# Optimization experiments

Hardware: AMD Instinct MI355X
Metric: run time of the kernel (lower is better)

## Reference

```python
import jax, jax.numpy as jnp
import numpy as np

LEAK = 0.2

def leaky(x):
    return jnp.where(x > 0, x, LEAK * x)

def relu(x):
    return jnp.maximum(x, 0)

def conv1d(x, w):
    # x [B,Cin,L], w [Cout,Cin,3], stride 1, padding 1
    return jax.lax.conv_general_dilated(x, w, (1,), [(1, 1)],
        dimension_numbers=('NCH', 'OIH', 'NCH'))

def conv2d(x, w, pad, dil=1, groups=1):
    return jax.lax.conv_general_dilated(x, w, (1, 1), [(pad, pad), (pad, pad)],
        rhs_dilation=(dil, dil), feature_group_count=groups,
        dimension_numbers=('NCHW', 'OIHW', 'NCHW'))

def bn2d(x, p, eps=1e-5):
    # p: [4,C] = gamma, beta, running_mean, running_var (eval-mode BN)
    g, b, m, v = p
    s = (1, -1, 1, 1)
    return (x - m.reshape(s)) * (g.reshape(s) / jnp.sqrt(v.reshape(s) + eps)) + b.reshape(s)

def layernorm(x, g, b, eps=1e-5):
    mu = x.mean(-1, keepdims=True)
    var = ((x - mu) ** 2).mean(-1, keepdims=True)
    return (x - mu) / jnp.sqrt(var + eps) * g + b

def l2n(x, axis, eps):
    n = jnp.sqrt((x * x).sum(axis, keepdims=True))
    return x / jnp.maximum(n, eps)


def setup_inputs() -> dict:
    key = jax.random.key(0)
    B, C, H, W = 4, 64, 48, 48
    D, Fn, T, V = 256, 8, 4, 16
    E = 16  # orthogonal prototype embed dim
    ks = iter(jax.random.split(key, 64))
    def rn(shape, s=0.05):
        return jax.random.normal(next(ks), shape, jnp.float32) * s
    def bnp(c):
        return jnp.stack([1.0 + rn((c,), 0.1), rn((c,), 0.1), rn((c,), 0.1), 1.0 + jnp.abs(rn((c,), 0.1))])
    return dict(
        basis_vector_bank=jax.random.normal(next(ks), (T, V, D), jnp.float32),
        task_f=jax.random.normal(next(ks), (B, C, 16, 16), jnp.float32),
        img_f=jax.random.normal(next(ks), (B, C, H, W), jnp.float32),
        protos=jax.random.normal(next(ks), (T, E), jnp.float32),
        tA_w1=rn((E // 4, 1, 3)), tA_w2=rn((E // 2, E // 4, 3)),
        iA_w=rn((E // 2, C, 3, 3)), iA_bn=bnp(E // 2),
        at_w1=rn((E, Fn // 2 * E)), at_b1=rn((Fn // 2 * E,)),
        at_ln_g=jnp.ones((Fn // 2 * E,)), at_ln_b=jnp.zeros((Fn // 2 * E,)),
        at_w2=rn((Fn // 2 * E, Fn * E)), at_b2=rn((Fn * E,)),
        bv_t1=rn((D // 4, 1, 3)), bv_t2=rn((D // 2, D // 4, 3)),
        bv_ic1=rn((D // 4, C, 3, 3)), bv_bn1=bnp(D // 4),
        bv_ic2=rn((D // 2, D // 4, 3, 3)), bv_bn2=bnp(D // 2),
        bv_w1=rn((D, D // 4)), bv_b1=rn((D // 4,)),
        bv_ln_g=jnp.ones((D // 4,)), bv_ln_b=jnp.zeros((D // 4,)),
        bv_w2=rn((D // 4, D)), bv_b2=rn((D,)),
        m1_w1=rn((D, D // 4)), m1_b1=rn((D // 4,)),
        m1_ln_g=jnp.ones((D // 4,)), m1_ln_b=jnp.zeros((D // 4,)),
        m1_w2=rn((D // 4, C * C)), m1_b2=rn((C * C,)),
        m3_w1=rn((D, D // 4)), m3_b1=rn((D // 4,)),
        m3_ln_g=jnp.ones((D // 4,)), m3_ln_b=jnp.zeros((D // 4,)),
        m3_w2=rn((D // 4, 9 * C * C)), m3_b2=rn((9 * C * C,)),
        blr_bn=bnp(C),
        zc_w=rn((C, C, 1, 1), 0.01), zc_b=rn((C,), 0.01),
    )


def _forward(basis_vector_bank, task_f, img_f, protos, tA_w1, tA_w2, iA_w, iA_bn,
             at_w1, at_b1, at_ln_g, at_ln_b, at_w2, at_b2,
             bv_t1, bv_t2, bv_ic1, bv_bn1, bv_ic2, bv_bn2,
             bv_w1, bv_b1, bv_ln_g, bv_ln_b, bv_w2, bv_b2,
             m1_w1, m1_b1, m1_ln_g, m1_ln_b, m1_w2, m1_b2,
             m3_w1, m3_b1, m3_ln_g, m3_ln_b, m3_w2, m3_b2,
             blr_bn, zc_w, zc_b):
    T, V, D = basis_vector_bank.shape
    B, C, H, W = img_f.shape
    E = protos.shape[1]
    Fn = at_w2.shape[1] // E
    tau = 0.5

    # --- A2SI routing features ---
    xt = task_f.reshape(B, 1, -1)
    t1 = conv1d(leaky(conv1d(xt, tA_w1)), tA_w2).mean(-1)          # [B,E/2]
    i1 = leaky(bn2d(conv2d(img_f, iA_w, 1), iA_bn)).mean((2, 3))   # [B,E/2]
    f1 = jnp.concatenate([t1, i1], axis=1)                         # [B,E]
    h = relu(layernorm(f1 @ at_w1 + at_b1, at_ln_g, at_ln_b))
    tif = (h @ at_w2 + at_b2).reshape(B, E, Fn)                    # [B,E,F]
    logits = jnp.einsum('te,bef->bft', l2n(protos, -1, 1e-8), l2n(tif, 1, 1e-8))  # [B,F,T]

    # hard gumbel-softmax (straight-through), fixed noise key for determinism
    u = jax.random.uniform(jax.random.key(42), logits.shape, jnp.float32, 1e-10, 1.0)
    g = -jnp.log(-jnp.log(u))
    y = jax.nn.softmax((logits + g) / tau, axis=-1)
    idx = jnp.argmax(y, axis=-1)                                   # [B,F]
    y_hard = jax.nn.one_hot(idx, T, dtype=y.dtype)
    set_type = y_hard + y - jax.lax.stop_gradient(y)

    bank_flat = basis_vector_bank.reshape(T, V * D)
    sbvb = jnp.einsum('bft,tk->bfk', set_type, bank_flat).reshape(B, Fn, V, D)

    # --- BasisV_filter: filter feature ---
    xt2 = task_f.reshape(B, C, -1)
    rms = jnp.sqrt((xt2 ** 2).mean((1, 2), keepdims=True))
    xt2 = (xt2 / (rms + 1e-8)).reshape(B, 1, -1)
    te = conv1d(leaky(conv1d(xt2, bv_t1)), bv_t2).mean(-1)         # [B,D/2]
    ie = leaky(bn2d(conv2d(img_f, bv_ic1, 1), bv_bn1))
    ie = leaky(bn2d(conv2d(ie, bv_ic2, 1), bv_bn2)).mean((2, 3))   # [B,D/2]
    ff = jnp.concatenate([te, ie], axis=1)                         # [B,D]
    ff = relu(layernorm(ff @ bv_w1 + bv_b1, bv_ln_g, bv_ln_b)) @ bv_w2 + bv_b2

    # --- per-(batch,type) group gather/top-k/scatter, vectorized ---
    # group bank = bank of first filter with that type (hard one-hot -> type's bank)
    occ = idx[:, None, :] == jnp.arange(T)[None, :, None]          # [B,T,F]
    first = jnp.argmax(occ, axis=-1)                               # [B,T]
    Bg = jnp.take_along_axis(sbvb, first[:, :, None, None], axis=1)  # [B,T,V,D]
    # all rows of Q within a group are identical (filter_f expanded over F),
    # so S.max(0) == cosine(ff[b], Bg[b,t])
    scores = jnp.einsum('bd,btvd->btv', l2n(ff, -1, 1e-12), l2n(Bg, -1, 1e-12))
    order = jnp.argsort(-scores, axis=-1)                          # [B,T,V] topk order
    lt = jnp.tril(jnp.ones((Fn, Fn), bool), -1)                    # j < i
    rank = ((idx[:, :, None] == idx[:, None, :]) & lt).sum(-1)     # position in group
    bidx = jnp.arange(B)[:, None]
    sel = order[bidx, idx, rank]                                   # [B,F]
    bvf = Bg[bidx, idx, sel]                                       # [B,F,D]

    # --- per-filter dynamic convolutions ---
    w1 = relu(layernorm(bvf @ m1_w1 + m1_b1, m1_ln_g, m1_ln_b)) @ m1_w2 + m1_b2
    w1 = w1.reshape(B, Fn, C, C)                                   # [B,F,out,in]
    w3 = relu(layernorm(bvf @ m3_w1 + m3_b1, m3_ln_g, m3_ln_b)) @ m3_w2 + m3_b2
    w3 = w3.reshape(B * Fn, C, C, 3, 3)

    dp0 = jnp.einsum('bfoc,bchw->bfohw', w1, img_f)                # 1x1 branch
    xin = jnp.broadcast_to(img_f[:, None], (B, Fn, C, H, W)).reshape(1, B * Fn * C, H, W)
    ker = w3.reshape(B * Fn * C, C, 3, 3)
    dpd = [conv2d(xin, ker, d, dil=d, groups=B * Fn).reshape(B, Fn, C, H, W)
           for d in (1, 2, 3)]                                     # same-padded dilated 3x3
    t_ = idx[:, :, None, None, None]
    dp = jnp.where(t_ == 0, dp0, jnp.where(t_ == 1, dpd[0],
         jnp.where(t_ == 2, dpd[1], dpd[2])))                      # [B,F,C,H,W]

    x = leaky(bn2d(dp.reshape(B * Fn, C, H, W), blr_bn)).reshape(B, Fn, C, H, W).mean(1)
    a = conv2d(x, zc_w, 0) + zc_b.reshape(1, -1, 1, 1)
    return a + img_f


@jax.jit
def reference(basis_vector_bank, task_f, img_f, protos, tA_w1, tA_w2, iA_w, iA_bn,
              at_w1, at_b1, at_ln_g, at_ln_b, at_w2, at_b2,
              bv_t1, bv_t2, bv_ic1, bv_bn1, bv_ic2, bv_bn2,
              bv_w1, bv_b1, bv_ln_g, bv_ln_b, bv_w2, bv_b2,
              m1_w1, m1_b1, m1_ln_g, m1_ln_b, m1_w2, m1_b2,
              m3_w1, m3_b1, m3_ln_g, m3_ln_b, m3_w2, m3_b2,
              blr_bn, zc_w, zc_b):
    return _forward(basis_vector_bank, task_f, img_f, protos, tA_w1, tA_w2, iA_w, iA_bn,
                    at_w1, at_b1, at_ln_g, at_ln_b, at_w2, at_b2,
                    bv_t1, bv_t2, bv_ic1, bv_bn1, bv_ic2, bv_bn2,
                    bv_w1, bv_b1, bv_ln_g, bv_ln_b, bv_w2, bv_b2,
                    m1_w1, m1_b1, m1_ln_g, m1_ln_b, m1_w2, m1_b2,
                    m3_w1, m3_b1, m3_ln_g, m3_ln_b, m3_w2, m3_b2,
                    blr_bn, zc_w, zc_b)
```

## Files before the change

kernel.cpp:

```cpp
#include <hip/hip_runtime.h>
#include <math.h>

#define LEAKC 0.2f

#define NB 4
#define NC 64
#define LLEN 16384
#define HW 2304
#define PP 54
#define PHW 2916
#define SLABP 72

typedef __attribute__((ext_vector_type(8))) short short8;
typedef __attribute__((ext_vector_type(4))) float floatx4;

__device__ __forceinline__ float leaky(float x){ return x > 0.f ? x : LEAKC*x; }

__device__ __forceinline__ float wave_sum64(float v){
  for(int off=32;off;off>>=1) v += __shfl_xor(v,off);
  return v;
}

__device__ __forceinline__ unsigned short f2bf(float x){
  unsigned u=__float_as_uint(x);
  unsigned r=u+0x7FFFu+((u>>16)&1u);
  return (unsigned short)(r>>16);
}

__device__ __forceinline__ void threefry2x32(unsigned k0, unsigned k1, unsigned& x0, unsigned& x1){
  unsigned ks0=k0, ks1=k1, ks2=k0^k1^0x1BD11BDAu;
  x0+=ks0; x1+=ks1;
  const int rot0[4]={13,15,26,6};
  const int rot1[4]={17,29,16,24};
#define TF_APPLY(rr) {for(int r=0;r<4;r++){x0+=x1; x1=(x1<<rr[r])|(x1>>(32-rr[r])); x1^=x0;}}
  TF_APPLY(rot0); x0+=ks1; x1+=ks2+1u;
  TF_APPLY(rot1); x0+=ks2; x1+=ks0+2u;
  TF_APPLY(rot0); x0+=ks0; x1+=ks1+3u;
  TF_APPLY(rot1); x0+=ks1; x1+=ks2+4u;
  TF_APPLY(rot0); x0+=ks2; x1+=ks0+5u;
#undef TF_APPLY
}

__device__ __forceinline__ float jax_uniform128(int i){
  unsigned x0=0u, x1=(unsigned)i;
  threefry2x32(0u,42u,x0,x1);
  unsigned bits = x0 ^ x1;
  unsigned fb=(bits>>9)|0x3f800000u;
  float f=__uint_as_float(fb)-1.0f;
  float u=f*(1.0f-1e-10f)+1e-10f;
  return fmaxf(1e-10f,u);
}

__global__ __launch_bounds__(256) void k_pre(const float* __restrict__ task_f,
                      const float* __restrict__ w1A, const float* __restrict__ w1B,
                      float* __restrict__ totA, float* __restrict__ a0A, float* __restrict__ aLA,
                      float* __restrict__ totB, float* __restrict__ a0B, float* __restrict__ aLB,
                      float* __restrict__ rmsacc,
                      const float* __restrict__ img,
                      const float* __restrict__ w1, const float* __restrict__ w2,
                      const float* __restrict__ wa,
                      unsigned short* __restrict__ imgTP,
                      unsigned short* __restrict__ W1T, unsigned short* __restrict__ W2T,
                      unsigned short* __restrict__ WAT,
                      const float* __restrict__ mw1, const float* __restrict__ mw3,
                      const float* __restrict__ bvw1p, const float* __restrict__ bvw2p,
                      const float* __restrict__ bvt2p, const float* __restrict__ atw2p,
                      const float* __restrict__ bankp, float* __restrict__ warm){
  if(blockIdx.x<256){
    int b=blockIdx.x>>6, seg=blockIdx.x&63;
    const float* x=task_f+b*LLEN;
    float tA[4]={0,0,0,0};
    float tB[64];
#pragma unroll
    for(int c=0;c<64;c++) tB[c]=0.f;
    float sq=0.f;
    int l=seg*256+threadIdx.x;
    {
      float xm=(l>0)?x[l-1]:0.f;
      float xc=x[l];
      float xp=(l<LLEN-1)?x[l+1]:0.f;
      sq=xc*xc;
#pragma unroll
      for(int c=0;c<4;c++){
        float a=leaky(w1A[c*3+0]*xm + w1A[c*3+1]*xc + w1A[c*3+2]*xp);
        tA[c]=a;
        if(l==0) a0A[b*4+c]=a;
        if(l==LLEN-1) aLA[b*4+c]=a;
      }
#pragma unroll
      for(int c=0;c<64;c++){
        float a=leaky(w1B[c*3+0]*xm + w1B[c*3+1]*xc + w1B[c*3+2]*xp);
        tB[c]=a;
        if(l==0) a0B[b*64+c]=a;
        if(l==LLEN-1) aLB[b*64+c]=a;
      }
    }
    sq=wave_sum64(sq);
#pragma unroll
    for(int c=0;c<4;c++) tA[c]=wave_sum64(tA[c]);
#pragma unroll
    for(int c=0;c<64;c++){
      float v=tB[c];
      for(int off=32;off;off>>=1) v+=__shfl_down(v,off);
      tB[c]=v;
    }
    __shared__ float redB[4][64];
    __shared__ float redA[4][4];
    __shared__ float redQ[4];
    int wave=threadIdx.x>>6, lane=threadIdx.x&63;
    if(lane==0){
#pragma unroll
      for(int c=0;c<64;c++) redB[wave][c]=tB[c];
#pragma unroll
      for(int c=0;c<4;c++) redA[wave][c]=tA[c];
      redQ[wave]=sq;
    }
    __syncthreads();
    if(threadIdx.x<64){
      float s=redB[0][threadIdx.x]+redB[1][threadIdx.x]+redB[2][threadIdx.x]+redB[3][threadIdx.x];
      atomicAdd(&totB[b*64+threadIdx.x], s);
    } else if(threadIdx.x<68){
      int c=threadIdx.x-64;
      float s=redA[0][c]+redA[1][c]+redA[2][c]+redA[3][c];
      atomicAdd(&totA[b*4+c], s);
    } else if(threadIdx.x==68){
      atomicAdd(&rmsacc[b], redQ[0]+redQ[1]+redQ[2]+redQ[3]);
    }
  } else if(blockIdx.x<400){
    int blk=blockIdx.x-256;
    int b=blk/36, t=blk%36;
    int p0=t*64;
    __shared__ float tile[64][65];
    int pp=threadIdx.x&63, c4=threadIdx.x>>6;
    for(int r=0;r<16;r++){
      int c=c4*16+r;
      tile[c][pp]=img[(b*64+c)*HW + p0+pp];
    }
    __syncthreads();
    int pxl=threadIdx.x>>2, cg=(threadIdx.x&3)*16;
    unsigned out[8];
#pragma unroll
    for(int q=0;q<8;q++){
      unsigned lo=f2bf(tile[cg+2*q][pxl]);
      unsigned hi=f2bf(tile[cg+2*q+1][pxl]);
      out[q]=lo|(hi<<16);
    }
    int px=p0+pxl;
    int h=px/48, w=px-h*48;
    int poff=(h+3)*PP+(w+3);
    unsigned* dst=(unsigned*)(imgTP + ((size_t)(b*PHW+poff))*64 + cg);
#pragma unroll
    for(int q=0;q<8;q++) dst[q]=out[q];
  } else if(blockIdx.x<868){
    int n=(blockIdx.x-400)*256+threadIdx.x;
    if(n<9*64*64){
      int tap=n>>12, oc=(n>>6)&63, c=n&63;
      W1T[n]=f2bf(w1[oc*576+c*9+tap]);
    } else if(n<9*64*64+9*128*64){
      int m=n-9*64*64;
      int tap=m/8192, r=m-tap*8192, oc=r>>6, c=r&63;
      W2T[m]=f2bf(w2[oc*576+c*9+tap]);
    } else {
      int q=n-9*64*64-9*128*64;
      if(q<9*16*64){
        int tap=q>>10, r=q&1023, o=r>>6, c=r&63;
        WAT[q]=(o<8)?f2bf(wa[o*576+c*9+tap]):(unsigned short)0;
      }
    }
  } else {
    int t=(blockIdx.x-868)*256+threadIdx.x;
    float a=0.f;
    for(int i=t;i*16<16384;i+=4096) a+=mw1[i*16];
    for(int i=t;i*16<16384;i+=4096) a+=mw3[i*16];
    for(int i=t;i*16<16384;i+=4096) a+=bvw1p[i*16];
    for(int i=t;i*16<16384;i+=4096) a+=bvw2p[i*16];
    for(int i=t;i*16<24576;i+=4096) a+=bvt2p[i*16];
    for(int i=t;i*16<8192;i+=4096) a+=atw2p[i*16];
    for(int i=t;i*16<16384;i+=4096) a+=bankp[i*16];
    warm[t&1023]=a;
  }
}

__global__ __launch_bounds__(256) void k_conv1(const unsigned short* __restrict__ imgTP,
                        const unsigned short* __restrict__ W1T,
                        const unsigned short* __restrict__ WAT,
                        const float* __restrict__ bn1, const float* __restrict__ bnA,
                        unsigned short* __restrict__ ie1TP, float* __restrict__ i1){
  int lane=threadIdx.x&63, mt=threadIdx.x>>6;
  int n0=lane&15, kg=lane>>4;
  if(blockIdx.x<96){
    int blk=blockIdx.x;
    int b=blk/24, hp=blk-b*24;
    int h0=hp*2;
    __shared__ unsigned short slab[4*54*SLABP];
    {
      const unsigned short* ibase=imgTP+((size_t)b*PHW+(size_t)(h0+2)*PP)*64;
      for(int e=threadIdx.x;e<4*54*8;e+=256){
        int rr=e/(54*8), rem=e-rr*54*8, w=rem>>3, ck=rem&7;
        uint4 v=*(const uint4*)(ibase+((size_t)(rr*PP+w))*64+ck*8);
        *(uint4*)(slab+(rr*54+w)*SLABP+ck*8)=v;
      }
    }
    __syncthreads();
    floatx4 acc[6];
#pragma unroll
    for(int i=0;i<6;i++) acc[i]=(floatx4){0.f,0.f,0.f,0.f};
#pragma unroll
    for(int ti=0;ti<3;ti++){
#pragma unroll
      for(int tj=0;tj<3;tj++){
        int tap=ti*3+tj;
        const unsigned short* Ab=W1T+(size_t)tap*4096;
#pragma unroll
        for(int c0=0;c0<64;c0+=32){
          short8 a=*(const short8*)(Ab+((mt*16+n0)*64+c0+kg*8));
#pragma unroll
          for(int rr=0;rr<2;rr++){
            int sr=rr+ti;
#pragma unroll
            for(int wc=0;wc<3;wc++){
              int wp=wc*16+n0+tj+2;
              short8 bv=*(const short8*)(slab+(sr*54+wp)*SLABP+c0+kg*8);
              acc[rr*3+wc]=__builtin_amdgcn_mfma_f32_16x16x32_bf16(a,bv,acc[rr*3+wc],0,0,0);
            }
          }
        }
      }
    }
    int obase=mt*16+kg*4;
    float scale[4],m_[4],be_[4];
#pragma unroll
    for(int reg=0;reg<4;reg++){
      int o=obase+reg;
      scale[reg]=bn1[o]/sqrtf(bn1[192+o]+1e-5f);
      m_[reg]=bn1[128+o]; be_[reg]=bn1[64+o];
    }
#pragma unroll
    for(int rr=0;rr<2;rr++){
#pragma unroll
      for(int wc=0;wc<3;wc++){
        int poff=(h0+rr+3)*PP + wc*16+n0+3;
        float v0=leaky((acc[rr*3+wc][0]-m_[0])*scale[0]+be_[0]);
        float v1=leaky((acc[rr*3+wc][1]-m_[1])*scale[1]+be_[1]);
        float v2=leaky((acc[rr*3+wc][2]-m_[2])*scale[2]+be_[2]);
        float v3=leaky((acc[rr*3+wc][3]-m_[3])*scale[3]+be_[3]);
        unsigned w0=f2bf(v0)|((unsigned)f2bf(v1)<<16);
        unsigned w1=f2bf(v2)|((unsigned)f2bf(v3)<<16);
        uint2 pk={w0,w1};
        *(uint2*)(ie1TP+((size_t)(b*PHW+poff)*64+obase))=pk;
      }
    }
  } else {
    int blk=blockIdx.x-96;
    int b=blk/6, hg=blk%6;
    int hp=hg*4+mt;
    int h0=hp*2;
    const unsigned short* ib=imgTP+(size_t)b*PHW*64;
    floatx4 acc[6];
#pragma unroll
    for(int i=0;i<6;i++) acc[i]=(floatx4){0.f,0.f,0.f,0.f};
#pragma unroll
    for(int ti=0;ti<3;ti++){
#pragma unroll
      for(int tj=0;tj<3;tj++){
        int tap=ti*3+tj;
        const unsigned short* Ab=WAT+(size_t)tap*1024;
#pragma unroll
        for(int c0=0;c0<64;c0+=32){
          short8 a=*(const short8*)(Ab+(n0*64+c0+kg*8));
#pragma unroll
          for(int rr=0;rr<2;rr++){
            int r=h0+rr+ti-1+3;
#pragma unroll
            for(int wc=0;wc<3;wc++){
              int w=wc*16+n0+tj-1+3;
              short8 bv=*(const short8*)(ib+((size_t)(r*PP+w)*64+c0+kg*8));
              acc[rr*3+wc]=__builtin_amdgcn_mfma_f32_16x16x32_bf16(a,bv,acc[rr*3+wc],0,0,0);
            }
          }
        }
      }
    }
    int obase=kg*4;
#pragma unroll
    for(int reg=0;reg<4;reg++){
      int o=obase+reg;
      float part=0;
      if(o<8){
        float scale=bnA[o]/sqrtf(bnA[24+o]+1e-5f);
        float m_=bnA[16+o], be_=bnA[8+o];
#pragma unroll
        for(int i=0;i<6;i++) part+=leaky((acc[i][reg]-m_)*scale+be_);
      }
      for(int off=1;off<16;off<<=1) part+=__shfl_xor(part,off);
      if(n0==0 && o<8) atomicAdd(&i1[b*8+o], part*(1.f/2304.f));
    }
  }
}

__global__ __launch_bounds__(512) void k_ic2M(const unsigned short* __restrict__ ie1TP,
                       const unsigned short* __restrict__ W2T,
                       const float* __restrict__ bn, float* __restrict__ ie){
  int blk=blockIdx.x;
  int b=blk/24, hp=blk-b*24;
  int tid=threadIdx.x;
  int lane=tid&63, mt=tid>>6;
  int n0=lane&15, kg=lane>>4;
  int h0=hp*2;
  __shared__ unsigned short slab[4*54*SLABP];
  {
    const unsigned short* ibase=ie1TP+((size_t)b*PHW+(size_t)(h0+2)*PP)*64;
    for(int e=tid;e<4*54*8;e+=512){
      int rr=e/(54*8), rem=e-rr*54*8, w=rem>>3, ck=rem&7;
      uint4 v=*(const uint4*)(ibase+((size_t)(rr*PP+w))*64+ck*8);
      *(uint4*)(slab+(rr*54+w)*SLABP+ck*8)=v;
    }
  }
  __syncthreads();
  floatx4 acc[6];
#pragma unroll
  for(int i=0;i<6;i++) acc[i]=(floatx4){0.f,0.f,0.f,0.f};
#pragma unroll
  for(int ti=0;ti<3;ti++){
#pragma unroll
    for(int tj=0;tj<3;tj++){
      int tap=ti*3+tj;
      const unsigned short* Ab=W2T+(size_t)tap*8192;
#pragma unroll
      for(int c0=0;c0<64;c0+=32){
        short8 a=*(const short8*)(Ab+((mt*16+n0)*64+c0+kg*8));
#pragma unroll
        for(int rr=0;rr<2;rr++){
          int sr=rr+ti;
#pragma unroll
          for(int wc=0;wc<3;wc++){
            int wp=wc*16+n0+tj+2;
            short8 bv=*(const short8*)(slab+(sr*54+wp)*SLABP+c0+kg*8);
            acc[rr*3+wc]=__builtin_amdgcn_mfma_f32_16x16x32_bf16(a,bv,acc[rr*3+wc],0,0,0);
          }
        }
      }
    }
  }
  int obase=mt*16+kg*4;
#pragma unroll
  for(int reg=0;reg<4;reg++){
    int o=obase+reg;
    float scale=bn[o]/sqrtf(bn[384+o]+1e-5f);
    float m_=bn[256+o], be_=bn[128+o];
    float part=0;
#pragma unroll
    for(int i=0;i<6;i++) part+=leaky((acc[i][reg]-m_)*scale+be_);
    for(int off=1;off<16;off<<=1) part+=__shfl_xor(part,off);
    if(n0==0) atomicAdd(&ie[b*128+o], part*(1.f/2304.f));
  }
}

__global__ __launch_bounds__(512,1) void k_mid(
    const float* __restrict__ totA, const float* __restrict__ a0A, const float* __restrict__ aLA,
    const float* __restrict__ totB, const float* __restrict__ a0B, const float* __restrict__ aLB,
    const float* __restrict__ rmsacc,
    const float* __restrict__ tA_w2, const float* __restrict__ bv_t2,
    const float* __restrict__ i1, const float* __restrict__ ie,
    const float* __restrict__ at_w1, const float* __restrict__ at_b1,
    const float* __restrict__ at_ln_g, const float* __restrict__ at_ln_b,
    const float* __restrict__ at_w2, const float* __restrict__ at_b2,
    const float* __restrict__ protos,
    const float* __restrict__ bv_w1, const float* __restrict__ bv_b1,
    const float* __restrict__ bv_ln_g, const float* __restrict__ bv_ln_b,
    const float* __restrict__ bv_w2, const float* __restrict__ bv_b2,
    const float* __restrict__ bank,
    const float* __restrict__ m1_w1, const float* __restrict__ m1_b1,
    const float* __restrict__ m1_g,  const float* __restrict__ m1_bb,
    const float* __restrict__ m3_w1, const float* __restrict__ m3_b1,
    const float* __restrict__ m3_g,  const float* __restrict__ m3_bb,
    int* __restrict__ idxo, float* __restrict__ hid1, float* __restrict__ hid3){
  int b=blockIdx.x;
  int tid=threadIdx.x;
  int lane=tid&63, wv=tid>>6;
  const float invL=1.0f/16384.0f;
  __shared__ float sT[64], s0[64], sL[64];
  __shared__ float part[512];
  __shared__ float te_s[128], t1_s[8];
  __shared__ float f1[16], h[64], tif[128], tifn[128], tden[8], pden[4], pn[64], z[32];
  __shared__ int sidx[8], sfirst[4], srank[8], rows[8];
  __shared__ float fbuf[256], hh[64], ffn_s[256], finv_s;
  __shared__ float scores[64];
  __shared__ int order[64];
  __shared__ float bvf[2048];

  if(tid<64){ sT[tid]=totB[b*64+tid]; s0[tid]=a0B[b*64+tid]; sL[tid]=aLB[b*64+tid]; }
  __syncthreads();
  float scB=1.0f/(sqrtf(rmsacc[b]*invL)+1e-8f);
  if(tid<256){
    int c2=tid&127, h2=tid>>7;
    const float* wr=bv_t2+c2*192;
    float s=0;
    for(int c1=h2*32;c1<h2*32+32;c1+=8){
      float4 q[6];
      const float4* r4=(const float4*)(wr+c1*3);
#pragma unroll
      for(int u=0;u<6;u++) q[u]=r4[u];
      const float* qq=(const float*)q;
#pragma unroll
      for(int u=0;u<8;u++){
        int c=c1+u;
        float T=sT[c], A0=s0[c], AL=sL[c];
        s += qq[u*3+0]*(T-AL) + qq[u*3+1]*T + qq[u*3+2]*(T-A0);
      }
    }
    part[tid]=s;
  } else if(tid>=384 && tid<392){
    int c2=tid-384;
    float s=0;
    for(int c1=0;c1<4;c1++){
      float T=totA[b*4+c1], A0=a0A[b*4+c1], AL=aLA[b*4+c1];
      const float* w=&tA_w2[(c2*4+c1)*3];
      s += w[0]*(T-AL) + w[1]*T + w[2]*(T-A0);
    }
    t1_s[c2]=s*invL;
  }
  __syncthreads();
  if(tid<128) te_s[tid]=(part[tid]+part[tid+128])*invL*scB;
  __syncthreads();

  if(tid<8) f1[tid]=t1_s[tid];
  else if(tid<16) f1[tid]=i1[b*8+tid-8];
  __syncthreads();
  if(tid<64){
    float s=at_b1[lane];
#pragma unroll
    for(int i=0;i<16;i++) s+=f1[i]*at_w1[i*64+lane];
    float mu=wave_sum64(s)*(1.f/64.f);
    float d=s-mu;
    float var=wave_sum64(d*d)*(1.f/64.f);
    h[lane]=fmaxf(d*(1.0f/sqrtf(var+1e-5f))*at_ln_g[lane]+at_ln_b[lane],0.f);
  }
  __syncthreads();
  if(tid<256){
    int n=tid&127, h2=tid>>7;
    float a0=0,a1=0;
    for(int k=h2*32;k<h2*32+32;k+=2){
      a0+=h[k]*at_w2[k*128+n];
      a1+=h[k+1]*at_w2[(k+1)*128+n];
    }
    part[tid]=a0+a1;
  }
  __syncthreads();
  if(tid<128) tif[tid]=at_b2[tid]+part[tid]+part[tid+128];
  __syncthreads();
  if(tid<8){
    int f=tid;
    float ss=0; for(int e=0;e<16;e++){float v=tif[e*8+f]; ss+=v*v;}
    tden[f]=fmaxf(sqrtf(ss),1e-8f);
  } else if(tid<12){
    int t=tid-8;
    float ss=0; for(int e=0;e<16;e++){float v=protos[t*16+e]; ss+=v*v;}
    pden[t]=fmaxf(sqrtf(ss),1e-8f);
  }
  __syncthreads();
  if(tid<128) tifn[tid]=tif[tid]/tden[tid&7];
  if(tid<64) pn[tid]=protos[tid]/pden[tid>>4];
  __syncthreads();
  if(tid<32){
    int f=tid>>2, t=tid&3;
    float ss=0;
#pragma unroll
    for(int e=0;e<16;e++) ss+=pn[t*16+e]*tifn[e*8+f];
    float u=jax_uniform128(b*32+f*4+t);
    float g=-logf(-logf(u));
    z[tid]=ss+g;
  }
  __syncthreads();
  if(tid<8){
    float best=z[tid*4]; int bi=0;
    for(int t=1;t<4;t++){ float v=z[tid*4+t]; if(v>best){best=v;bi=t;} }
    sidx[tid]=bi;
  }
  __syncthreads();
  if(tid<4){
    int t=tid;
    int fi=0;
    for(int f=7;f>=0;f--) if(sidx[f]==t) fi=f;
    sfirst[t]=fi;
  } else if(tid<12){
    int f=tid-4;
    int c=0; for(int f2=0;f2<f;f2++) if(sidx[f2]==sidx[f]) c++;
    srank[f]=c;
  }
  __syncthreads();

  if(tid<128) fbuf[tid]=te_s[tid];
  else if(tid<256) fbuf[tid]=ie[b*128+tid-128];
  __syncthreads();
  if(tid<256){
    int l64=tid&63, q=tid>>6;
    float a0=0,a1=0,a2=0,a3=0;
    for(int k=q*64;k<q*64+64;k+=4){
      a0+=fbuf[k]  *bv_w1[k*64+l64];
      a1+=fbuf[k+1]*bv_w1[(k+1)*64+l64];
      a2+=fbuf[k+2]*bv_w1[(k+2)*64+l64];
      a3+=fbuf[k+3]*bv_w1[(k+3)*64+l64];
    }
    part[tid]=((a0+a1)+(a2+a3));
  }
  __syncthreads();
  if(tid<64){
    float s=bv_b1[lane]+part[lane]+part[64+lane]+part[128+lane]+part[192+lane];
    float mu=wave_sum64(s)*(1.f/64.f);
    float d=s-mu;
    float var=wave_sum64(d*d)*(1.f/64.f);
    hh[lane]=fmaxf(d*(1.0f/sqrtf(var+1e-5f))*bv_ln_g[lane]+bv_ln_b[lane],0.f);
  }
  __syncthreads();
  {
    int n=tid&255, h2=tid>>8;
    float a0=0,a1=0;
    for(int k=h2*32;k<h2*32+32;k+=2){
      a0+=hh[k]*bv_w2[k*256+n];
      a1+=hh[k+1]*bv_w2[(k+1)*256+n];
    }
    part[tid]=a0+a1;
  }
  __syncthreads();
  if(tid<256) ffn_s[tid]=bv_b2[tid]+part[tid]+part[tid+256];
  __syncthreads();
  if(tid<64){
    float sq=0;
#pragma unroll
    for(int u=0;u<4;u++){ float v=ffn_s[u*64+lane]; sq+=v*v; }
    sq=wave_sum64(sq);
    if(lane==0) finv_s=1.0f/fmaxf(sqrtf(sq),1e-12f);
  }
  __syncthreads();
  if(tid<256) ffn_s[tid]*=finv_s;
  __syncthreads();

  if(tid<128){
    int it=tid&63, h2=tid>>6;
    int t=it>>4, v=it&15;
    int tt=sidx[sfirst[t]];
    const float4* row=(const float4*)(bank+(tt*16+v)*256);
    float sa=0,na=0;
    for(int d4=h2*32;d4<h2*32+32;d4++){
      float4 r=row[d4];
      const float* fp=&ffn_s[d4*4];
      sa+=fp[0]*r.x+fp[1]*r.y+fp[2]*r.z+fp[3]*r.w;
      na+=r.x*r.x+r.y*r.y+r.z*r.z+r.w*r.w;
    }
    part[tid]=sa;
    part[256+tid]=na;
  }
  __syncthreads();
  if(tid<64) scores[tid]=(part[tid]+part[tid+64])/fmaxf(sqrtf(part[256+tid]+part[320+tid]),1e-12f);
  __syncthreads();
  if(tid<4){
    const float* sc=&scores[tid*16];
    unsigned used=0;
    for(int pk=0;pk<16;pk++){
      int best=-1; float bv=-1e30f;
      for(int v2=0;v2<16;v2++){
        if(used&(1u<<v2)) continue;
        float vv=sc[v2];
        if(best<0||vv>bv){bv=vv;best=v2;}
      }
      used|=1u<<best;
      order[tid*16+pk]=best;
    }
  }
  __syncthreads();
  if(tid<8){
    int t=sidx[tid];
    int v=order[t*16+srank[tid]];
    rows[tid]=t*16+v;
    idxo[b*8+tid]=t;
  }
  __syncthreads();

  for(int ii=tid;ii<2048;ii+=512){
    int r=ii>>8, d=ii&255;
    bvf[ii]=bank[rows[r]*256+d];
  }
  __syncthreads();
  {
    int r=wv;
    const float* bp=&bvf[r*256];
    float a0=0,a1=0,a2=0,a3=0;
    float c0=0,c1=0,c2=0,c3=0;
    for(int d=0;d<256;d+=4){
      float b0=bp[d],b1=bp[d+1],b2=bp[d+2],b3=bp[d+3];
      a0+=b0*m1_w1[d*64+lane];
      a1+=b1*m1_w1[(d+1)*64+lane];
      a2+=b2*m1_w1[(d+2)*64+lane];
      a3+=b3*m1_w1[(d+3)*64+lane];
      c0+=b0*m3_w1[d*64+lane];
      c1+=b1*m3_w1[(d+1)*64+lane];
      c2+=b2*m3_w1[(d+2)*64+lane];
      c3+=b3*m3_w1[(d+3)*64+lane];
    }
    float s1=m1_b1[lane]+((a0+a1)+(a2+a3));
    float s3=m3_b1[lane]+((c0+c1)+(c2+c3));
    float mu=wave_sum64(s1)*(1.f/64.f);
    float dd=s1-mu;
    float var=wave_sum64(dd*dd)*(1.f/64.f);
    hid1[(b*8+r)*64+lane]=fmaxf(dd*(1.0f/sqrtf(var+1e-5f))*m1_g[lane]+m1_bb[lane],0.f);
    mu=wave_sum64(s3)*(1.f/64.f);
    dd=s3-mu;
    var=wave_sum64(dd*dd)*(1.f/64.f);
    hid3[(b*8+r)*64+lane]=fmaxf(dd*(1.0f/sqrtf(var+1e-5f))*m3_g[lane]+m3_bb[lane],0.f);
  }
}

__global__ __launch_bounds__(256) void k_heads(const float* __restrict__ hid1, const float* __restrict__ hid3,
                        const float* __restrict__ w2a, const float* __restrict__ b2a,
                        const float* __restrict__ w2b, const float* __restrict__ b2b,
                        unsigned short* __restrict__ A1, unsigned short* __restrict__ A3){
  __shared__ float hl[2048];
  if(blockIdx.x<16){
    int n=blockIdx.x*256+threadIdx.x;
    for(int i=threadIdx.x;i<2048;i+=256) hl[i]=hid1[i];
    __syncthreads();
    float wcol[64];
#pragma unroll
    for(int k=0;k<64;k++) wcol[k]=w2a[k*4096+n];
    float bb=b2a[n];
    for(int bf=0;bf<32;bf++){
      float s=bb;
#pragma unroll
      for(int k=0;k<64;k++) s+=hl[bf*64+k]*wcol[k];
      A1[bf*4096+n]=f2bf(s);
    }
  } else {
    int n=(blockIdx.x-16)*256+threadIdx.x;
    for(int i=threadIdx.x;i<2048;i+=256) hl[i]=hid3[i];
    __syncthreads();
    float wcol[64];
#pragma unroll
    for(int k=0;k<64;k++) wcol[k]=w2b[(size_t)k*36864+n];
    float bb=b2b[n];
    int o=n/576, rem=n-o*576;
    int c=rem/9, tap=rem-c*9;
    size_t base=((size_t)tap*64+o)*64+c;
    for(int bf=0;bf<32;bf++){
      float s=bb;
#pragma unroll
      for(int k=0;k<64;k++) s+=hl[bf*64+k]*wcol[k];
      A3[(size_t)bf*9*4096+base]=f2bf(s);
    }
  }
}

__global__ __launch_bounds__(512) void k_dynF(const unsigned short* __restrict__ imgTP,
                       const unsigned short* __restrict__ A1, const unsigned short* __restrict__ A3,
                       const int* __restrict__ idx, const float* __restrict__ bn,
                       const float* __restrict__ zc_w, const float* __restrict__ zc_b,
                       const float* __restrict__ img, float* __restrict__ out){
  int blk=blockIdx.x;
  int b=blk/48, r0=blk-b*48;
  int tid=threadIdx.x;
  int lane=tid&63, w8=tid>>6;
  int mt=w8&3, fh=w8>>2;
  int n0=lane&15, kg=lane>>4;
  __shared__ unsigned short slab[7*54*SLABP];
  __shared__ float xl[64*50];
  __shared__ float zl[4096];
  for(int i=tid;i<4096;i+=512) zl[i]=zc_w[i];
  for(int i=tid;i<3200;i+=512) xl[i]=0.f;
  {
    const unsigned short* ibase=imgTP+((size_t)b*PHW+(size_t)r0*PP)*64;
    for(int e=tid;e<7*54*8;e+=512){
      int rr=e/(54*8), rem=e-rr*54*8, w=rem>>3, ck=rem&7;
      uint4 v=*(const uint4*)(ibase + ((size_t)(rr*PP+w))*64 + ck*8);
      *(uint4*)(slab + (rr*54+w)*SLABP + ck*8)=v;
    }
  }
  __syncthreads();
  int obase=mt*16+kg*4;
  float scale[4],m_[4],be_[4];
#pragma unroll
  for(int reg=0;reg<4;reg++){
    int o=obase+reg;
    scale[reg]=bn[o]/sqrtf(bn[192+o]+1e-5f);
    m_[reg]=bn[128+o]; be_[reg]=bn[64+o];
  }
  float xsum[3][4];
#pragma unroll
  for(int wc=0;wc<3;wc++)
#pragma unroll
    for(int reg=0;reg<4;reg++) xsum[wc][reg]=0.f;
  for(int f=fh*4;f<fh*4+4;f++){
    int bf=b*8+f;
    int tt=idx[bf];
    floatx4 acc[3];
#pragma unroll
    for(int i=0;i<3;i++) acc[i]=(floatx4){0.f,0.f,0.f,0.f};
    if(tt==0){
      const unsigned short* Ab=A1+(size_t)bf*4096;
#pragma unroll
      for(int c0=0;c0<64;c0+=32){
        short8 a=*(const short8*)(Ab+((mt*16+n0)*64+c0+kg*8));
#pragma unroll
        for(int wc=0;wc<3;wc++){
          short8 bv=*(const short8*)(slab + (3*54 + wc*16+n0+3)*SLABP + c0+kg*8);
          acc[wc]=__builtin_amdgcn_mfma_f32_16x16x32_bf16(a,bv,acc[wc],0,0,0);
        }
      }
    } else {
      int d=tt;
      const unsigned short* A3b=A3+(size_t)bf*9*4096;
#pragma unroll
      for(int ti=0;ti<3;ti++){
        int lr=d*(ti-1)+3;
#pragma unroll
        for(int tj=0;tj<3;tj++){
          int tap=ti*3+tj;
          int dw=d*(tj-1)+3;
          const unsigned short* Ab=A3b+(size_t)tap*4096;
#pragma unroll
          for(int c0=0;c0<64;c0+=32){
            short8 a=*(const short8*)(Ab+((mt*16+n0)*64+c0+kg*8));
#pragma unroll
            for(int wc=0;wc<3;wc++){
              short8 bv=*(const short8*)(slab + (lr*54 + wc*16+n0+dw)*SLABP + c0+kg*8);
              acc[wc]=__builtin_amdgcn_mfma_f32_16x16x32_bf16(a,bv,acc[wc],0,0,0);
            }
          }
        }
      }
    }
#pragma unroll
    for(int wc=0;wc<3;wc++)
#pragma unroll
      for(int reg=0;reg<4;reg++)
        xsum[wc][reg]+=leaky((acc[wc][reg]-m_[reg])*scale[reg]+be_[reg]);
  }
#pragma unroll
  for(int wc=0;wc<3;wc++)
#pragma unroll
    for(int reg=0;reg<4;reg++)
      atomicAdd(&xl[(obase+reg)*50 + wc*16+n0], xsum[wc][reg]*0.125f);
  __syncthreads();
  size_t base=(size_t)b*64*HW + r0*48;
  for(int e=tid;e<3072;e+=512){
    int o=e/48, px=e-o*48;
    float s=zc_b[o];
#pragma unroll
    for(int c=0;c<64;c++) s+=zl[o*64+c]*xl[c*50+px];
    size_t a=base+(size_t)o*HW+px;
    out[a]=s+img[a];
  }
}

extern "C" void kernel_launch(void* const* d_in, const int* in_sizes, int n_in,
                              void* d_out, int out_size, void* d_ws, size_t ws_size,
                              hipStream_t stream){
  const float* bank   =(const float*)d_in[0];
  const float* task_f =(const float*)d_in[1];
  const float* img_f  =(const float*)d_in[2];
  const float* protos =(const float*)d_in[3];
  const float* tA_w1  =(const float*)d_in[4];
  const float* tA_w2  =(const float*)d_in[5];
  const float* iA_w   =(const float*)d_in[6];
  const float* iA_bn  =(const float*)d_in[7];
  const float* at_w1  =(const float*)d_in[8];
  const float* at_b1  =(const float*)d_in[9];
  const float* at_ln_g=(const float*)d_in[10];
  const float* at_ln_b=(const float*)d_in[11];
  const float* at_w2  =(const float*)d_in[12];
  const float* at_b2  =(const float*)d_in[13];
  const float* bv_t1  =(const float*)d_in[14];
  const float* bv_t2  =(const float*)d_in[15];
  const float* bv_ic1 =(const float*)d_in[16];
  const float* bv_bn1 =(const float*)d_in[17];
  const float* bv_ic2 =(const float*)d_in[18];
  const float* bv_bn2 =(const float*)d_in[19];
  const float* bv_w1  =(const float*)d_in[20];
  const float* bv_b1  =(const float*)d_in[21];
  const float* bv_ln_g=(const float*)d_in[22];
  const float* bv_ln_b=(const float*)d_in[23];
  const float* bv_w2  =(const float*)d_in[24];
  const float* bv_b2  =(const float*)d_in[25];
  const float* m1_w1  =(const float*)d_in[26];
  const float* m1_b1  =(const float*)d_in[27];
  const float* m1_ln_g=(const float*)d_in[28];
  const float* m1_ln_b=(const float*)d_in[29];
  const float* m1_w2  =(const float*)d_in[30];
  const float* m1_b2  =(const float*)d_in[31];
  const float* m3_w1  =(const float*)d_in[32];
  const float* m3_b1  =(const float*)d_in[33];
  const float* m3_ln_g=(const float*)d_in[34];
  const float* m3_ln_b=(const float*)d_in[35];
  const float* m3_w2  =(const float*)d_in[36];
  const float* m3_b2  =(const float*)d_in[37];
  const float* blr_bn =(const float*)d_in[38];
  const float* zc_w   =(const float*)d_in[39];
  const float* zc_b   =(const float*)d_in[40];

  float* ws=(float*)d_ws;
  float* totA=ws+0;       float* a0A=ws+16;      float* aLA=ws+32;
  float* totB=ws+48;      float* a0B=ws+304;     float* aLB=ws+560;
  float* rmsacc=ws+816;   float* i1 =ws+820;     float* ie =ws+852;
  int*   idxp  =(int*)(ws+2932);
  float* hid1=ws+3044;    float* hid3=ws+5092;
  unsigned short* A1p  =(unsigned short*)(ws+7140);
  unsigned short* A3p  =(unsigned short*)(ws+72676);
  unsigned short* imgTP=(unsigned short*)(ws+662500);
  unsigned short* ie1TP=(unsigned short*)(ws+1035748);
  unsigned short* W1Tp =(unsigned short*)(ws+1408996);
  unsigned short* W2Tp =(unsigned short*)(ws+1427428);
  unsigned short* WATp =(unsigned short*)(ws+1464292);
  float* warm =ws+1468900;

  hipMemsetAsync(ws, 0, 1364*sizeof(float), stream);
  hipMemsetAsync(imgTP, 0, 2*746496*sizeof(unsigned short), stream);

  k_pre<<<884,256,0,stream>>>(task_f, tA_w1, bv_t1,
                              totA, a0A, aLA, totB, a0B, aLB, rmsacc,
                              img_f, bv_ic1, bv_ic2, iA_w, imgTP, W1Tp, W2Tp, WATp,
                              m1_w1, m3_w1, bv_w1, bv_w2, bv_t2, at_w2, bank, warm);
  k_conv1<<<120,256,0,stream>>>(imgTP, W1Tp, WATp, bv_bn1, iA_bn, ie1TP, i1);
  k_ic2M<<<96,512,0,stream>>>(ie1TP, W2Tp, bv_bn2, ie);
  k_mid<<<4,512,0,stream>>>(totA,a0A,aLA,totB,a0B,aLB, rmsacc, tA_w2, bv_t2, i1, ie,
                            at_w1, at_b1, at_ln_g, at_ln_b, at_w2, at_b2, protos,
                            bv_w1, bv_b1, bv_ln_g, bv_ln_b, bv_w2, bv_b2, bank,
                            m1_w1, m1_b1, m1_ln_g, m1_ln_b,
                            m3_w1, m3_b1, m3_ln_g, m3_ln_b,
                            idxp, hid1, hid3);
  k_heads<<<160,256,0,stream>>>(hid1, hid3, m1_w2, m1_b2, m3_w2, m3_b2, A1p, A3p);
  k_dynF<<<192,512,0,stream>>>(imgTP, A1p, A3p, idxp, blr_bn, zc_w, zc_b, img_f, (float*)d_out);

  (void)in_sizes; (void)n_in; (void)out_size; (void)ws_size;
}
```

Before: 284.4 us.

## Fuse two conv stages in LDS and replace atomics with partial-sum buffers

Merges the first and second 3x3 convolutions into one kernel. The intermediate activation stays in shared memory with a one-row halo that is recomputed per block, so the global ie1TP round trip and one launch go away. Atomic accumulations in k_pre and the conv kernels become per-block partial writes that k_mid sums, which removes both hipMemsetAsync calls. Only the imgTP padding border is zeroed, by extra blocks inside k_pre. The cost is about 50% redundant conv1 work for the halo rows, fewer blocks for the second conv, and serial reductions added to k_mid.

```diff
diff --git a/kernel.cpp b/kernel.cpp
--- a/kernel.cpp
+++ b/kernel.cpp
@@ -10,6 +10,8 @@
 #define PP 54
 #define PHW 2916
 #define SLABP 72
+#define CP 72
+#define IE1C 50
 
 typedef __attribute__((ext_vector_type(8))) short short8;
 typedef __attribute__((ext_vector_type(4))) float floatx4;
@@ -53,9 +55,9 @@
 
 __global__ __launch_bounds__(256) void k_pre(const float* __restrict__ task_f,
                       const float* __restrict__ w1A, const float* __restrict__ w1B,
-                      float* __restrict__ totA, float* __restrict__ a0A, float* __restrict__ aLA,
-                      float* __restrict__ totB, float* __restrict__ a0B, float* __restrict__ aLB,
-                      float* __restrict__ rmsacc,
+                      float* __restrict__ totApart, float* __restrict__ a0A, float* __restrict__ aLA,
+                      float* __restrict__ totBpart, float* __restrict__ a0B, float* __restrict__ aLB,
+                      float* __restrict__ rmspart,
                       const float* __restrict__ img,
                       const float* __restrict__ w1, const float* __restrict__ w2,
                       const float* __restrict__ wa,
@@ -118,13 +120,12 @@
     __syncthreads();
     if(threadIdx.x<64){
       float s=redB[0][threadIdx.x]+redB[1][threadIdx.x]+redB[2][threadIdx.x]+redB[3][threadIdx.x];
-      atomicAdd(&totB[b*64+threadIdx.x], s);
+      totBpart[(size_t)(b*64+seg)*64+threadIdx.x]=s;
     } else if(threadIdx.x<68){
       int c=threadIdx.x-64;
-      float s=redA[0][c]+redA[1][c]+redA[2][c]+redA[3][c];
-      atomicAdd(&totA[b*4+c], s);
+      totApart[(b*64+seg)*4+c]=redA[0][c]+redA[1][c]+redA[2][c]+redA[3][c];
     } else if(threadIdx.x==68){
-      atomicAdd(&rmsacc[b], redQ[0]+redQ[1]+redQ[2]+redQ[3]);
+      rmspart[b*64+seg]=redQ[0]+redQ[1]+redQ[2]+redQ[3];
     }
   } else if(blockIdx.x<400){
     int blk=blockIdx.x-256;
@@ -167,7 +168,7 @@
         WAT[q]=(o<8)?f2bf(wa[o*576+c*9+tap]):(unsigned short)0;
       }
     }
-  } else {
+  } else if(blockIdx.x<884){
     int t=(blockIdx.x-868)*256+threadIdx.x;
     float a=0.f;
     for(int i=t;i*16<16384;i+=4096) a+=mw1[i*16];
@@ -178,82 +179,148 @@
     for(int i=t;i*16<8192;i+=4096) a+=atw2p[i*16];
     for(int i=t;i*16<16384;i+=4096) a+=bankp[i*16];
     warm[t&1023]=a;
-  }
-}
-
-__global__ __launch_bounds__(256) void k_conv1(const unsigned short* __restrict__ imgTP,
+  } else {
+    int id=(blockIdx.x-884)*256+threadIdx.x;
+    uint4 z=make_uint4(0,0,0,0);
+    for(int cch=id;cch<19584;cch+=4096){
+      int ck=cch&7, pxid=cch>>3;
+      int b=pxid/612, p=pxid-b*612;
+      int h,w;
+      if(p<324){ int r=p/54; w=p-r*54; h=(r<3)?r:(r+48); }
+      else { int q=p-324; int r2=q/6; int cc=q-r2*6; h=3+r2; w=(cc<3)?cc:(cc+48); }
+      *(uint4*)(imgTP + ((size_t)(b*PHW + h*PP + w))*64 + ck*8)=z;
+    }
+  }
+}
+
+__global__ __launch_bounds__(512) void k_conv12(const unsigned short* __restrict__ imgTP,
                         const unsigned short* __restrict__ W1T,
+                        const unsigned short* __restrict__ W2T,
                         const unsigned short* __restrict__ WAT,
-                        const float* __restrict__ bn1, const float* __restrict__ bnA,
-                        unsigned short* __restrict__ ie1TP, float* __restrict__ i1){
-  int lane=threadIdx.x&63, mt=threadIdx.x>>6;
+                        const float* __restrict__ bn1, const float* __restrict__ bn2,
+                        const float* __restrict__ bnA,
+                        float* __restrict__ iepart, float* __restrict__ i1part){
+  int tid=threadIdx.x;
+  int lane=tid&63, wv=tid>>6;
   int n0=lane&15, kg=lane>>4;
   if(blockIdx.x<96){
     int blk=blockIdx.x;
     int b=blk/24, hp=blk-b*24;
     int h0=hp*2;
-    __shared__ unsigned short slab[4*54*SLABP];
+    __shared__ unsigned short slab[6*54*SLABP];
+    __shared__ unsigned short ie1[4*IE1C*CP];
     {
-      const unsigned short* ibase=imgTP+((size_t)b*PHW+(size_t)(h0+2)*PP)*64;
-      for(int e=threadIdx.x;e<4*54*8;e+=256){
+      const unsigned short* ibase=imgTP+((size_t)b*PHW+(size_t)(h0+1)*PP)*64;
+      for(int e=tid;e<6*54*8;e+=512){
         int rr=e/(54*8), rem=e-rr*54*8, w=rem>>3, ck=rem&7;
         uint4 v=*(const uint4*)(ibase+((size_t)(rr*PP+w))*64+ck*8);
         *(uint4*)(slab+(rr*54+w)*SLABP+ck*8)=v;
       }
+      if(tid<64){
+        int br=tid>>4, cq=(tid>>3)&1, ck=tid&7;
+        *(uint4*)(ie1+((size_t)(br*IE1C+(cq?49:0)))*CP+ck*8)=make_uint4(0,0,0,0);
+      }
     }
     __syncthreads();
-    floatx4 acc[6];
-#pragma unroll
-    for(int i=0;i<6;i++) acc[i]=(floatx4){0.f,0.f,0.f,0.f};
-#pragma unroll
-    for(int ti=0;ti<3;ti++){
-#pragma unroll
-      for(int tj=0;tj<3;tj++){
-        int tap=ti*3+tj;
-        const unsigned short* Ab=W1T+(size_t)tap*4096;
-#pragma unroll
-        for(int c0=0;c0<64;c0+=32){
-          short8 a=*(const short8*)(Ab+((mt*16+n0)*64+c0+kg*8));
-#pragma unroll
-          for(int rr=0;rr<2;rr++){
-            int sr=rr+ti;
-#pragma unroll
-            for(int wc=0;wc<3;wc++){
-              int wp=wc*16+n0+tj+2;
-              short8 bv=*(const short8*)(slab+(sr*54+wp)*SLABP+c0+kg*8);
-              acc[rr*3+wc]=__builtin_amdgcn_mfma_f32_16x16x32_bf16(a,bv,acc[rr*3+wc],0,0,0);
+    {
+      int mt=wv&3, rh=wv>>2;
+      floatx4 acc[2][3];
+#pragma unroll
+      for(int rr=0;rr<2;rr++)
+#pragma unroll
+        for(int nt=0;nt<3;nt++) acc[rr][nt]=(floatx4){0.f,0.f,0.f,0.f};
+#pragma unroll
+      for(int ti=0;ti<3;ti++){
+#pragma unroll
+        for(int tj=0;tj<3;tj++){
+          int tap=ti*3+tj;
+          const unsigned short* Ab=W1T+(size_t)tap*4096;
+#pragma unroll
+          for(int c0=0;c0<64;c0+=32){
+            short8 a=*(const short8*)(Ab+((mt*16+n0)*64+c0+kg*8));
+#pragma unroll
+            for(int rr=0;rr<2;rr++){
+              int sr=rh*2+rr+ti;
+#pragma unroll
+              for(int nt=0;nt<3;nt++){
+                int sc=nt*16+n0+tj+2;
+                short8 bv=*(const short8*)(slab+(sr*54+sc)*SLABP+c0+kg*8);
+                acc[rr][nt]=__builtin_amdgcn_mfma_f32_16x16x32_bf16(a,bv,acc[rr][nt],0,0,0);
+              }
             }
           }
         }
       }
-    }
-    int obase=mt*16+kg*4;
-    float scale[4],m_[4],be_[4];
-#pragma unroll
-    for(int reg=0;reg<4;reg++){
-      int o=obase+reg;
-      scale[reg]=bn1[o]/sqrtf(bn1[192+o]+1e-5f);
-      m_[reg]=bn1[128+o]; be_[reg]=bn1[64+o];
-    }
-#pragma unroll
-    for(int rr=0;rr<2;rr++){
-#pragma unroll
-      for(int wc=0;wc<3;wc++){
-        int poff=(h0+rr+3)*PP + wc*16+n0+3;
-        float v0=leaky((acc[rr*3+wc][0]-m_[0])*scale[0]+be_[0]);
-        float v1=leaky((acc[rr*3+wc][1]-m_[1])*scale[1]+be_[1]);
-        float v2=leaky((acc[rr*3+wc][2]-m_[2])*scale[2]+be_[2]);
-        float v3=leaky((acc[rr*3+wc][3]-m_[3])*scale[3]+be_[3]);
-        unsigned w0=f2bf(v0)|((unsigned)f2bf(v1)<<16);
-        unsigned w1=f2bf(v2)|((unsigned)f2bf(v3)<<16);
-        uint2 pk={w0,w1};
-        *(uint2*)(ie1TP+((size_t)(b*PHW+poff)*64+obase))=pk;
+      int obase=mt*16+kg*4;
+      float scale[4],m_[4],be_[4];
+#pragma unroll
+      for(int reg=0;reg<4;reg++){
+        int o=obase+reg;
+        scale[reg]=bn1[o]/sqrtf(bn1[192+o]+1e-5f);
+        m_[reg]=bn1[128+o]; be_[reg]=bn1[64+o];
+      }
+#pragma unroll
+      for(int rr=0;rr<2;rr++){
+        int br=rh*2+rr;
+        bool rv=((unsigned)(h0-1+br))<48u;
+#pragma unroll
+        for(int nt=0;nt<3;nt++){
+          float v0=rv?leaky((acc[rr][nt][0]-m_[0])*scale[0]+be_[0]):0.f;
+          float v1=rv?leaky((acc[rr][nt][1]-m_[1])*scale[1]+be_[1]):0.f;
+          float v2=rv?leaky((acc[rr][nt][2]-m_[2])*scale[2]+be_[2]):0.f;
+          float v3=rv?leaky((acc[rr][nt][3]-m_[3])*scale[3]+be_[3]):0.f;
+          unsigned w0=f2bf(v0)|((unsigned)f2bf(v1)<<16);
+          unsigned w1=f2bf(v2)|((unsigned)f2bf(v3)<<16);
+          uint2 pk={w0,w1};
+          *(uint2*)(ie1+((size_t)(br*IE1C+(nt*16+1+n0)))*CP+obase)=pk;
+        }
+      }
+    }
+    __syncthreads();
+    {
+      int mt2=wv;
+      floatx4 acc[6];
+#pragma unroll
+      for(int i=0;i<6;i++) acc[i]=(floatx4){0.f,0.f,0.f,0.f};
+#pragma unroll
+      for(int ti=0;ti<3;ti++){
+#pragma unroll
+        for(int tj=0;tj<3;tj++){
+          int tap=ti*3+tj;
+          const unsigned short* Ab=W2T+(size_t)tap*8192;
+#pragma unroll
+          for(int c0=0;c0<64;c0+=32){
+            short8 a=*(const short8*)(Ab+((mt2*16+n0)*64+c0+kg*8));
+#pragma unroll
+            for(int rr=0;rr<2;rr++){
+              int sr=rr+ti;
+#pragma unroll
+              for(int wc=0;wc<3;wc++){
+                int q=wc*16+n0+tj;
+                short8 bv=*(const short8*)(ie1+((size_t)(sr*IE1C+q))*CP+c0+kg*8);
+                acc[rr*3+wc]=__builtin_amdgcn_mfma_f32_16x16x32_bf16(a,bv,acc[rr*3+wc],0,0,0);
+              }
+            }
+          }
+        }
+      }
+      int obase=mt2*16+kg*4;
+#pragma unroll
+      for(int reg=0;reg<4;reg++){
+        int o=obase+reg;
+        float scale=bn2[o]/sqrtf(bn2[384+o]+1e-5f);
+        float m_=bn2[256+o], be_=bn2[128+o];
+        float part=0;
+#pragma unroll
+        for(int i=0;i<6;i++) part+=leaky((acc[i][reg]-m_)*scale+be_);
+        for(int off=1;off<16;off<<=1) part+=__shfl_xor(part,off);
+        if(n0==0) iepart[(b*24+hp)*128+o]=part*(1.f/2304.f);
       }
     }
   } else {
-    int blk=blockIdx.x-96;
-    int b=blk/6, hg=blk%6;
-    int hp=hg*4+mt;
+    int blk2=blockIdx.x-96;
+    int b=blk2/3, hg=blk2-b*3;
+    int hp=hg*8+wv;
     int h0=hp*2;
     const unsigned short* ib=imgTP+(size_t)b*PHW*64;
     floatx4 acc[6];
@@ -293,75 +360,17 @@
         for(int i=0;i<6;i++) part+=leaky((acc[i][reg]-m_)*scale+be_);
       }
       for(int off=1;off<16;off<<=1) part+=__shfl_xor(part,off);
-      if(n0==0 && o<8) atomicAdd(&i1[b*8+o], part*(1.f/2304.f));
-    }
-  }
-}
-
-__global__ __launch_bounds__(512) void k_ic2M(const unsigned short* __restrict__ ie1TP,
-                       const unsigned short* __restrict__ W2T,
-                       const float* __restrict__ bn, float* __restrict__ ie){
-  int blk=blockIdx.x;
-  int b=blk/24, hp=blk-b*24;
-  int tid=threadIdx.x;
-  int lane=tid&63, mt=tid>>6;
-  int n0=lane&15, kg=lane>>4;
-  int h0=hp*2;
-  __shared__ unsigned short slab[4*54*SLABP];
-  {
-    const unsigned short* ibase=ie1TP+((size_t)b*PHW+(size_t)(h0+2)*PP)*64;
-    for(int e=tid;e<4*54*8;e+=512){
-      int rr=e/(54*8), rem=e-rr*54*8, w=rem>>3, ck=rem&7;
-      uint4 v=*(const uint4*)(ibase+((size_t)(rr*PP+w))*64+ck*8);
-      *(uint4*)(slab+(rr*54+w)*SLABP+ck*8)=v;
-    }
-  }
-  __syncthreads();
-  floatx4 acc[6];
-#pragma unroll
-  for(int i=0;i<6;i++) acc[i]=(floatx4){0.f,0.f,0.f,0.f};
-#pragma unroll
-  for(int ti=0;ti<3;ti++){
-#pragma unroll
-    for(int tj=0;tj<3;tj++){
-      int tap=ti*3+tj;
-      const unsigned short* Ab=W2T+(size_t)tap*8192;
-#pragma unroll
-      for(int c0=0;c0<64;c0+=32){
-        short8 a=*(const short8*)(Ab+((mt*16+n0)*64+c0+kg*8));
-#pragma unroll
-        for(int rr=0;rr<2;rr++){
-          int sr=rr+ti;
-#pragma unroll
-          for(int wc=0;wc<3;wc++){
-            int wp=wc*16+n0+tj+2;
-            short8 bv=*(const short8*)(slab+(sr*54+wp)*SLABP+c0+kg*8);
-            acc[rr*3+wc]=__builtin_amdgcn_mfma_f32_16x16x32_bf16(a,bv,acc[rr*3+wc],0,0,0);
-          }
-        }
-      }
-    }
-  }
-  int obase=mt*16+kg*4;
-#pragma unroll
-  for(int reg=0;reg<4;reg++){
-    int o=obase+reg;
-    float scale=bn[o]/sqrtf(bn[384+o]+1e-5f);
-    float m_=bn[256+o], be_=bn[128+o];
-    float part=0;
-#pragma unroll
-    for(int i=0;i<6;i++) part+=leaky((acc[i][reg]-m_)*scale+be_);
-    for(int off=1;off<16;off<<=1) part+=__shfl_xor(part,off);
-    if(n0==0) atomicAdd(&ie[b*128+o], part*(1.f/2304.f));
+      if(n0==0 && o<8) i1part[(b*24+hp)*8+o]=part*(1.f/2304.f);
+    }
   }
 }
 
 __global__ __launch_bounds__(512,1) void k_mid(
-    const float* __restrict__ totA, const float* __restrict__ a0A, const float* __restrict__ aLA,
-    const float* __restrict__ totB, const float* __restrict__ a0B, const float* __restrict__ aLB,
-    const float* __restrict__ rmsacc,
+    const float* __restrict__ totApart, const float* __restrict__ a0A, const float* __restrict__ aLA,
+    const float* __restrict__ totBpart, const float* __restrict__ a0B, const float* __restrict__ aLB,
+    const float* __restrict__ rmspart,
     const float* __restrict__ tA_w2, const float* __restrict__ bv_t2,
-    const float* __restrict__ i1, const float* __restrict__ ie,
+    const float* __restrict__ i1part, const float* __restrict__ iepart,
     const float* __restrict__ at_w1, const float* __restrict__ at_b1,
     const float* __restrict__ at_ln_g, const float* __restrict__ at_ln_b,
     const float* __restrict__ at_w2, const float* __restrict__ at_b2,
@@ -380,6 +389,8 @@
   int lane=tid&63, wv=tid>>6;
   const float invL=1.0f/16384.0f;
   __shared__ float sT[64], s0[64], sL[64];
+  __shared__ float totA_s[4];
+  __shared__ float rms_s;
   __shared__ float part[512];
   __shared__ float te_s[128], t1_s[8];
   __shared__ float f1[16], h[64], tif[128], tifn[128], tden[8], pden[4], pn[64], z[32];
@@ -389,9 +400,29 @@
   __shared__ int order[64];
   __shared__ float bvf[2048];
 
-  if(tid<64){ sT[tid]=totB[b*64+tid]; s0[tid]=a0B[b*64+tid]; sL[tid]=aLB[b*64+tid]; }
-  __syncthreads();
-  float scB=1.0f/(sqrtf(rmsacc[b]*invL)+1e-8f);
+  if(tid<64){
+    float s=0;
+#pragma unroll 8
+    for(int seg=0;seg<64;seg++) s+=totBpart[(size_t)(b*64+seg)*64+tid];
+    sT[tid]=s;
+  } else if(tid<128){
+    int t=tid-64;
+    s0[t]=a0B[b*64+t]; sL[t]=aLB[b*64+t];
+  } else if(tid<192){
+    float v=rmspart[b*64+(tid-128)];
+    v=wave_sum64(v);
+    if(tid==128) rms_s=v;
+  } else if(tid<256){
+    int c=tid-192;
+    if(c<4){
+      float s=0;
+#pragma unroll 8
+      for(int seg=0;seg<64;seg++) s+=totApart[(b*64+seg)*4+c];
+      totA_s[c]=s;
+    }
+  }
+  __syncthreads();
+  float scB=1.0f/(sqrtf(rms_s*invL)+1e-8f);
   if(tid<256){
     int c2=tid&127, h2=tid>>7;
     const float* wr=bv_t2+c2*192;
@@ -414,7 +445,7 @@
     int c2=tid-384;
     float s=0;
     for(int c1=0;c1<4;c1++){
-      float T=totA[b*4+c1], A0=a0A[b*4+c1], AL=aLA[b*4+c1];
+      float T=totA_s[c1], A0=a0A[b*4+c1], AL=aLA[b*4+c1];
       const float* w=&tA_w2[(c2*4+c1)*3];
       s += w[0]*(T-AL) + w[1]*T + w[2]*(T-A0);
     }
@@ -425,7 +456,13 @@
   __syncthreads();
 
   if(tid<8) f1[tid]=t1_s[tid];
-  else if(tid<16) f1[tid]=i1[b*8+tid-8];
+  else if(tid<16){
+    int f=tid-8;
+    float s=0;
+#pragma unroll
+    for(int g=0;g<24;g++) s+=i1part[(b*24+g)*8+f];
+    f1[tid]=s;
+  }
   __syncthreads();
   if(tid<64){
     float s=at_b1[lane];
@@ -491,7 +528,13 @@
   __syncthreads();
 
   if(tid<128) fbuf[tid]=te_s[tid];
-  else if(tid<256) fbuf[tid]=ie[b*128+tid-128];
+  else if(tid<256){
+    int c=tid-128;
+    float s=0;
+#pragma unroll 8
+    for(int g=0;g<24;g++) s+=iepart[(b*24+g)*128+c];
+    fbuf[tid]=s;
+  }
   __syncthreads();
   if(tid<256){
     int l64=tid&63, q=tid>>6;
@@ -797,30 +840,34 @@
   const float* zc_b   =(const float*)d_in[40];
 
   float* ws=(float*)d_ws;
-  float* totA=ws+0;       float* a0A=ws+16;      float* aLA=ws+32;
-  float* totB=ws+48;      float* a0B=ws+304;     float* aLB=ws+560;
-  float* rmsacc=ws+816;   float* i1 =ws+820;     float* ie =ws+852;
-  int*   idxp  =(int*)(ws+2932);
-  float* hid1=ws+3044;    float* hid3=ws+5092;
-  unsigned short* A1p  =(unsigned short*)(ws+7140);
-  unsigned short* A3p  =(unsigned short*)(ws+72676);
-  unsigned short* imgTP=(unsigned short*)(ws+662500);
-  unsigned short* ie1TP=(unsigned short*)(ws+1035748);
-  unsigned short* W1Tp =(unsigned short*)(ws+1408996);
-  unsigned short* W2Tp =(unsigned short*)(ws+1427428);
-  unsigned short* WATp =(unsigned short*)(ws+1464292);
-  float* warm =ws+1468900;
-
-  hipMemsetAsync(ws, 0, 1364*sizeof(float), stream);
-  hipMemsetAsync(imgTP, 0, 2*746496*sizeof(unsigned short), stream);
-
-  k_pre<<<884,256,0,stream>>>(task_f, tA_w1, bv_t1,
-                              totA, a0A, aLA, totB, a0B, aLB, rmsacc,
+  float* totApart=ws+0;
+  float* a0A  =ws+1024;
+  float* aLA  =ws+1040;
+  float* totBpart=ws+1056;
+  float* a0B  =ws+17440;
+  float* aLB  =ws+17696;
+  float* rmspart=ws+17952;
+  float* i1part =ws+18208;
+  float* iepart =ws+18976;
+  int*   idxp   =(int*)(ws+31264);
+  float* hid1=ws+31296;
+  float* hid3=ws+33344;
+  unsigned short* A1p  =(unsigned short*)(ws+35392);
+  unsigned short* A3p  =(unsigned short*)(ws+100928);
+  unsigned short* imgTP=(unsigned short*)(ws+690752);
+  unsigned short* W1Tp =(unsigned short*)(ws+1064000);
+  unsigned short* W2Tp =(unsigned short*)(ws+1082432);
+  unsigned short* WATp =(unsigned short*)(ws+1119296);
+  float* warm =ws+1123904;
+
+  k_pre<<<900,256,0,stream>>>(task_f, tA_w1, bv_t1,
+                              totApart, a0A, aLA, totBpart, a0B, aLB, rmspart,
                               img_f, bv_ic1, bv_ic2, iA_w, imgTP, W1Tp, W2Tp, WATp,
                               m1_w1, m3_w1, bv_w1, bv_w2, bv_t2, at_w2, bank, warm);
-  k_conv1<<<120,256,0,stream>>>(imgTP, W1Tp, WATp, bv_bn1, iA_bn, ie1TP, i1);
-  k_ic2M<<<96,512,0,stream>>>(ie1TP, W2Tp, bv_bn2, ie);
-  k_mid<<<4,512,0,stream>>>(totA,a0A,aLA,totB,a0B,aLB, rmsacc, tA_w2, bv_t2, i1, ie,
+  k_conv12<<<108,512,0,stream>>>(imgTP, W1Tp, W2Tp, WATp, bv_bn1, bv_bn2, iA_bn,
+                                 iepart, i1part);
+  k_mid<<<4,512,0,stream>>>(totApart,a0A,aLA,totBpart,a0B,aLB, rmspart, tA_w2, bv_t2,
+                            i1part, iepart,
                             at_w1, at_b1, at_ln_g, at_ln_b, at_w2, at_b2, protos,
                             bv_w1, bv_b1, bv_ln_g, bv_ln_b, bv_w2, bv_b2, bank,
                             m1_w1, m1_b1, m1_ln_g, m1_ln_b,
```

Result: faster. 267.2 us (-6.0%).
